# Kernel tuning notes

Hardware: AMD Instinct MI355X
Metric: run time of the kernel (lower is better)

The kernel has to match this reference:

```python
import jax, jax.numpy as jnp
import numpy as np

SEQ, IN_DIM, OUT_DIM = 8192, 1024, 1024

def setup_inputs() -> dict:
    key = jax.random.key(0)
    k1, k2, k3, k4 = jax.random.split(key, 4)
    inputs = jax.random.normal(k1, (SEQ, IN_DIM), dtype=jnp.float32)
    # torch.nn.Linear stores weight as [out_dim, in_dim]; y = x @ W.T
    w_query = jax.random.normal(k2, (OUT_DIM, IN_DIM), dtype=jnp.float32) * (1.0 / np.sqrt(IN_DIM))
    w_key = jax.random.normal(k3, (OUT_DIM, IN_DIM), dtype=jnp.float32) * (1.0 / np.sqrt(IN_DIM))
    w_value = jax.random.normal(k4, (OUT_DIM, IN_DIM), dtype=jnp.float32) * (1.0 / np.sqrt(IN_DIM))
    return {"inputs": inputs, "w_query": w_query, "w_key": w_key, "w_value": w_value}

def reference(inputs, w_query, w_key, w_value):
    # QKV projections: [S, D_out]
    q = inputs @ w_query.T
    k = inputs @ w_key.T
    v = inputs @ w_value.T
    scale = 1.0 / jnp.sqrt(jnp.asarray(k.shape[-1], dtype=q.dtype))
    scores = (q @ k.T) * scale  # [S, S]
    # causal mask: lower-triangular kept, upper set to -inf
    s = scores.shape[0]
    causal = jnp.tril(jnp.ones((s, s), dtype=bool))
    scores = jnp.where(causal, scores, -jnp.inf)
    attn = jax.nn.softmax(scores, axis=-1)
    return attn @ v
```

## Files before the change

kernel.cpp:

```cpp
#include <hip/hip_runtime.h>
#include <stdint.h>
#include <stddef.h>


#define SEQ   8192
#define DIM   1024

typedef __bf16 bf16x8 __attribute__((ext_vector_type(8)));
typedef float  f32x4  __attribute__((ext_vector_type(4)));
typedef uint16_t u16x8 __attribute__((ext_vector_type(8)));

#define MFMA16(a, b, c) __builtin_amdgcn_mfma_f32_16x16x32_bf16((a), (b), (c), 0, 0, 0)

__device__ __forceinline__ uint16_t f2bf(float f) {
  uint32_t u = __builtin_bit_cast(uint32_t, f);
  return (uint16_t)((u + 0x7fffu + ((u >> 16) & 1u)) >> 16);
}
__device__ __forceinline__ float bf2f(uint16_t h) {
  uint32_t u = ((uint32_t)h) << 16;
  return __builtin_bit_cast(float, u);
}

typedef const __attribute__((address_space(1))) uint32_t* gas_t;
typedef __attribute__((address_space(3))) uint32_t* las_t;
__device__ __forceinline__ void async16(const void* g, void* l) {
  __builtin_amdgcn_global_load_lds((gas_t)g, (las_t)l, 16, 0, 0);
}


__global__ __launch_bounds__(256) void cast_f32_bf16(const float* __restrict__ src,
                                                     uint16_t* __restrict__ dst, int n) {
  int i = (blockIdx.x * 256 + threadIdx.x) * 4;
  if (i + 3 < n) {
    float4 v = *(const float4*)(src + i);
    ushort4 o;
    o.x = f2bf(v.x); o.y = f2bf(v.y); o.z = f2bf(v.z); o.w = f2bf(v.w);
    *(ushort4*)(dst + i) = o;
  }
}

__global__ __launch_bounds__(256) void qkv_gemm(const uint16_t* __restrict__ A,
                                                const uint16_t* __restrict__ B,
                                                uint16_t* __restrict__ Qblk,
                                                uint16_t* __restrict__ Kblk,
                                                uint16_t* __restrict__ Vb) {
  __shared__ __align__(16) uint16_t As[128][72];
  __shared__ __align__(16) uint16_t Bs[128][72];
  const int t    = threadIdx.x;
  const int w    = t >> 6;
  const int lane = t & 63;
  const int lm   = lane & 15;
  const int qd   = lane >> 4;
  const int wrow = (w >> 1) * 64;
  const int wcol = (w & 1) * 64;
  const int rowbase = blockIdx.y * 128;
  const int colbase = blockIdx.x * 128;

  f32x4 acc[4][4] = {};

  for (int kb = 0; kb < DIM; kb += 64) {
    __syncthreads();
#pragma unroll
    for (int rep = 0; rep < 4; ++rep) {
      int i = rep * 256 + t;
      int r = i >> 3, c8 = i & 7;
      *(uint4*)(&As[r][c8 * 8]) =
          *(const uint4*)(A + (size_t)(rowbase + r) * DIM + kb + c8 * 8);
    }
#pragma unroll
    for (int rep = 0; rep < 4; ++rep) {
      int i = rep * 256 + t;
      int r = i >> 3, c8 = i & 7;
      *(uint4*)(&Bs[r][c8 * 8]) =
          *(const uint4*)(B + (size_t)(colbase + r) * DIM + kb + c8 * 8);
    }
    __syncthreads();
#pragma unroll
    for (int kc = 0; kc < 2; ++kc) {
      bf16x8 af[4], bfr[4];
#pragma unroll
      for (int mt = 0; mt < 4; ++mt)
        af[mt] = *(const bf16x8*)(&As[wrow + mt * 16 + lm][kc * 32 + qd * 8]);
#pragma unroll
      for (int nt = 0; nt < 4; ++nt)
        bfr[nt] = *(const bf16x8*)(&Bs[wcol + nt * 16 + lm][kc * 32 + qd * 8]);
#pragma unroll
      for (int mt = 0; mt < 4; ++mt)
#pragma unroll
        for (int nt = 0; nt < 4; ++nt)
          acc[mt][nt] = MFMA16(af[mt], bfr[nt], acc[mt][nt]);
    }
  }

#pragma unroll
  for (int mt = 0; mt < 4; ++mt)
#pragma unroll
    for (int nt = 0; nt < 4; ++nt)
#pragma unroll
      for (int r = 0; r < 4; ++r) {
        int m = rowbase + wrow + mt * 16 + qd * 4 + r;
        int n = colbase + wcol + nt * 16 + lm;
        uint16_t v = f2bf(acc[mt][nt][r]);
        int nn = n & 1023;
        if (n < 2048) {
          size_t off = (((size_t)(m >> 4) * 32 + (nn >> 5)) * 64 +
                        ((nn >> 3) & 3) * 16 + (m & 15)) * 8 + (nn & 7);
          if (n < 1024) Qblk[off] = v; else Kblk[off] = v;
        } else {
          Vb[(size_t)m * DIM + nn] = v;
        }
      }
}

__global__ __launch_bounds__(256) void transpose_v(const uint16_t* __restrict__ Vb,
                                                   uint16_t* __restrict__ Vblk) {
  __shared__ __align__(16) uint16_t tile[64][72];
  const int t  = threadIdx.x;
  const int mb = blockIdx.x * 64;
  const int db = blockIdx.y * 64;
#pragma unroll
  for (int rep = 0; rep < 2; ++rep) {
    int i = rep * 256 + t;
    int r = i >> 3, c = (i & 7) * 8;
    *(uint4*)(&tile[r][c]) = *(const uint4*)(Vb + (size_t)(mb + r) * DIM + db + c);
  }
  __syncthreads();
#pragma unroll
  for (int rep = 0; rep < 2; ++rep) {
    int i = rep * 256 + t;
    int d = i >> 3, mq = (i & 7) * 8;
    u16x8 v;
#pragma unroll
    for (int u = 0; u < 8; ++u) v[u] = tile[mq + u][d];
    int dg = db + d, kg = mb + mq;
    size_t off = (((size_t)(dg >> 4) * 256 + (kg >> 5)) * 64 +
                  ((kg >> 3) & 3) * 16 + (dg & 15)) * 8;
    *(u16x8*)(Vblk + off) = v;
  }
}

__global__ __launch_bounds__(512, 2) void attn_kernel(const uint16_t* __restrict__ Qblk,
                                                      const uint16_t* __restrict__ Kblk,
                                                      const uint16_t* __restrict__ Vblk,
                                                      uint16_t* __restrict__ P0,
                                                      uint16_t* __restrict__ P1,
                                                      float* __restrict__ Mm,
                                                      float* __restrict__ Ll) {
  __shared__ __align__(16) uint16_t Qs[32768];
  __shared__ __align__(16) uint16_t Pb[8192];
  __shared__ float smax[32][8];
  __shared__ float lsum[32][8];
  __shared__ float mrow[32];

  const int t    = threadIdx.x;
  const int w    = t >> 6;
  const int lane = t & 63;
  const int lm   = lane & 15;
  const int qd   = lane >> 4;
  const int par  = blockIdx.x & 1;
  const int p    = blockIdx.x >> 1;
  const float c1 = 0.045084220027780106f;

#pragma unroll 1
  for (int half = 0; half < 2; ++half) {
    const int tt   = half ? 255 - p : p;
    const int row0 = tt * 32;
    const int jn   = (tt >> 3) + 1;

    __syncthreads();
#pragma unroll
    for (int i = 0; i < 8; ++i)
      async16(Qblk + ((size_t)(tt * 64 + w * 8 + i)) * 512 + lane * 8,
              Qs + (w * 8 + i) * 512);
    __syncthreads();

    float m_run[2][4], l_run[2][4];
#pragma unroll
    for (int mt = 0; mt < 2; ++mt)
#pragma unroll
      for (int r = 0; r < 4; ++r) { m_run[mt][r] = -1e30f; l_run[mt][r] = 0.0f; }
    f32x4 o_acc[2][8] = {};

#pragma unroll 1
    for (int jg = par; jg < jn; jg += 2) {
      f32x4 sacc[2][2] = {};
      const uint16_t* kbp = Kblk + ((size_t)(jg * 16 + w * 2) * 32) * 512 + lane * 8;
      const uint16_t* qsp = Qs + lane * 8;
#pragma unroll 4
      for (int kb = 0; kb < 32; ++kb) {
        bf16x8 qf0 = *(const bf16x8*)(qsp + kb * 512);
        bf16x8 qf1 = *(const bf16x8*)(qsp + (32 + kb) * 512);
        bf16x8 kf0 = *(const bf16x8*)(kbp + (size_t)kb * 512);
        bf16x8 kf1 = *(const bf16x8*)(kbp + (size_t)(32 + kb) * 512);
        sacc[0][0] = MFMA16(qf0, kf0, sacc[0][0]);
        sacc[1][0] = MFMA16(qf1, kf0, sacc[1][0]);
        sacc[0][1] = MFMA16(qf0, kf1, sacc[0][1]);
        sacc[1][1] = MFMA16(qf1, kf1, sacc[1][1]);
      }

      if (jg == jn - 1) {
#pragma unroll
        for (int mt = 0; mt < 2; ++mt)
#pragma unroll
          for (int nt = 0; nt < 2; ++nt)
#pragma unroll
            for (int r = 0; r < 4; ++r) {
              int col = jg * 256 + w * 32 + nt * 16 + lm;
              int row = row0 + mt * 16 + qd * 4 + r;
              if (col > row) sacc[mt][nt][r] = -1e30f;
            }
      }

#pragma unroll
      for (int mt = 0; mt < 2; ++mt)
#pragma unroll
        for (int r = 0; r < 4; ++r) {
          float v = fmaxf(sacc[mt][0][r], sacc[mt][1][r]);
          v = fmaxf(v, __shfl_xor(v, 1));
          v = fmaxf(v, __shfl_xor(v, 2));
          v = fmaxf(v, __shfl_xor(v, 4));
          v = fmaxf(v, __shfl_xor(v, 8));
          if (lm == 0) smax[mt * 16 + qd * 4 + r][w] = v;
        }
      __syncthreads();

      float alpha[2][4], psum[2][4];
#pragma unroll
      for (int mt = 0; mt < 2; ++mt)
#pragma unroll
        for (int r = 0; r < 4; ++r) {
          int rl = mt * 16 + qd * 4 + r;
          float4 g0 = *(const float4*)&smax[rl][0];
          float4 g1 = *(const float4*)&smax[rl][4];
          float gm = fmaxf(fmaxf(fmaxf(g0.x, g0.y), fmaxf(g0.z, g0.w)),
                           fmaxf(fmaxf(g1.x, g1.y), fmaxf(g1.z, g1.w)));
          float mn = fmaxf(m_run[mt][r], gm);
          alpha[mt][r] = exp2f((m_run[mt][r] - mn) * c1);
          m_run[mt][r] = mn;
          psum[mt][r] = 0.0f;
        }
#pragma unroll
      for (int mt = 0; mt < 2; ++mt)
#pragma unroll
        for (int nt = 0; nt < 2; ++nt)
#pragma unroll
          for (int r = 0; r < 4; ++r) {
            float pv = exp2f((sacc[mt][nt][r] - m_run[mt][r]) * c1);
            psum[mt][r] += pv;
            Pb[((mt * 8 + w) * 64 + (nt * 2 + (lm >> 3)) * 16 + qd * 4 + r) * 8 + (lm & 7)] =
                f2bf(pv);
          }
#pragma unroll
      for (int mt = 0; mt < 2; ++mt)
#pragma unroll
        for (int r = 0; r < 4; ++r) {
          float s2 = psum[mt][r];
          s2 += __shfl_xor(s2, 1);
          s2 += __shfl_xor(s2, 2);
          s2 += __shfl_xor(s2, 4);
          s2 += __shfl_xor(s2, 8);
          l_run[mt][r] = l_run[mt][r] * alpha[mt][r] + s2;
        }
      __syncthreads();

#pragma unroll
      for (int mt = 0; mt < 2; ++mt)
#pragma unroll
        for (int dt = 0; dt < 8; ++dt)
#pragma unroll
          for (int r = 0; r < 4; ++r)
            o_acc[mt][dt][r] *= alpha[mt][r];

      const uint16_t* vbp = Vblk + ((size_t)(w * 8) * 256 + jg * 8) * 512 + lane * 8;
#pragma unroll 2
      for (int kc = 0; kc < 8; ++kc) {
        bf16x8 pf0 = *(const bf16x8*)(Pb + (kc * 64 + lane) * 8);
        bf16x8 pf1 = *(const bf16x8*)(Pb + ((8 + kc) * 64 + lane) * 8);
#pragma unroll
        for (int dt = 0; dt < 8; ++dt) {
          bf16x8 vf = *(const bf16x8*)(vbp + ((size_t)dt * 256 + kc) * 512);
          o_acc[0][dt] = MFMA16(pf0, vf, o_acc[0][dt]);
          o_acc[1][dt] = MFMA16(pf1, vf, o_acc[1][dt]);
        }
      }
    }

    if (lm == 0) {
#pragma unroll
      for (int mt = 0; mt < 2; ++mt)
#pragma unroll
        for (int r = 0; r < 4; ++r) {
          int rl = mt * 16 + qd * 4 + r;
          lsum[rl][w] = l_run[mt][r];
          if (w == 0) mrow[rl] = m_run[mt][r];
        }
    }
    __syncthreads();
    if (t < 32) {
      float4 a0 = *(const float4*)&lsum[t][0];
      float4 a1 = *(const float4*)&lsum[t][4];
      Mm[par * SEQ + row0 + t] = mrow[t];
      Ll[par * SEQ + row0 + t] = (a0.x + a0.y + a0.z + a0.w) + (a1.x + a1.y + a1.z + a1.w);
    }
    uint16_t* Pp = par ? P1 : P0;
#pragma unroll
    for (int mt = 0; mt < 2; ++mt)
#pragma unroll
      for (int dt = 0; dt < 8; ++dt)
#pragma unroll
        for (int r = 0; r < 4; ++r) {
          int row = row0 + mt * 16 + qd * 4 + r;
          int d   = w * 128 + dt * 16 + lm;
          Pp[(size_t)row * DIM + d] = f2bf(o_acc[mt][dt][r]);
        }
  }
}

__global__ __launch_bounds__(256) void merge_kernel(const uint16_t* __restrict__ P0,
                                                    const uint16_t* __restrict__ P1,
                                                    const float* __restrict__ Mm,
                                                    const float* __restrict__ Ll,
                                                    float* __restrict__ out) {
  const int row = blockIdx.x;
  const int d0  = threadIdx.x * 4;
  const float c1 = 0.045084220027780106f;
  float m0 = Mm[row], m1 = Mm[SEQ + row];
  float l0 = Ll[row], l1 = Ll[SEQ + row];
  float m  = fmaxf(m0, m1);
  float a0 = exp2f((m0 - m) * c1);
  float a1 = exp2f((m1 - m) * c1);
  float inv = 1.0f / (a0 * l0 + a1 * l1);
  ushort4 p0 = *(const ushort4*)(P0 + (size_t)row * DIM + d0);
  ushort4 p1 = *(const ushort4*)(P1 + (size_t)row * DIM + d0);
  float4 o;
  o.x = (a0 * bf2f(p0.x) + a1 * bf2f(p1.x)) * inv;
  o.y = (a0 * bf2f(p0.y) + a1 * bf2f(p1.y)) * inv;
  o.z = (a0 * bf2f(p0.z) + a1 * bf2f(p1.z)) * inv;
  o.w = (a0 * bf2f(p0.w) + a1 * bf2f(p1.w)) * inv;
  *(float4*)(out + (size_t)row * DIM + d0) = o;
}

extern "C" void kernel_launch(void* const* d_in, const int* in_sizes, int n_in,
                              void* d_out, int out_size, void* d_ws, size_t ws_size,
                              hipStream_t stream) {
  (void)in_sizes; (void)n_in; (void)out_size; (void)ws_size;
  const float* x  = (const float*)d_in[0];
  const float* wq = (const float*)d_in[1];
  const float* wk = (const float*)d_in[2];
  const float* wv = (const float*)d_in[3];
  float* out = (float*)d_out;

  char* ws = (char*)d_ws;
  uint16_t* Qblk = (uint16_t*)(ws);
  uint16_t* Kblk = (uint16_t*)(ws + 16777216);
  uint16_t* Vblk = (uint16_t*)(ws + 33554432);
  uint16_t* Vb   = (uint16_t*)(ws + 50331648);
  uint16_t* P0   = (uint16_t*)(ws + 50331648);
  uint16_t* xb   = (uint16_t*)(ws + 67108864);
  uint16_t* P1   = (uint16_t*)(ws + 67108864);
  uint16_t* wcat = (uint16_t*)(ws + 83886080);
  float*    Mm   = (float*)(ws + 83886080);
  float*    Ll   = (float*)(ws + 83886080 + 65536);

  cast_f32_bf16<<<8192, 256, 0, stream>>>(x,  xb,                   SEQ * DIM);
  cast_f32_bf16<<<1024, 256, 0, stream>>>(wq, wcat,                 DIM * DIM);
  cast_f32_bf16<<<1024, 256, 0, stream>>>(wk, wcat + DIM * DIM,     DIM * DIM);
  cast_f32_bf16<<<1024, 256, 0, stream>>>(wv, wcat + 2 * DIM * DIM, DIM * DIM);

  qkv_gemm<<<dim3(24, 64), 256, 0, stream>>>(xb, wcat, Qblk, Kblk, Vb);
  transpose_v<<<dim3(SEQ / 64, DIM / 64), 256, 0, stream>>>(Vb, Vblk);
  attn_kernel<<<256, 512, 0, stream>>>(Qblk, Kblk, Vblk, P0, P1, Mm, Ll);
  merge_kernel<<<SEQ, 256, 0, stream>>>(P0, P1, Mm, Ll, out);
}
```

Before: 557.6 us.

## Swizzle async LDS loads in QKV GEMM and halve attention P buffer

The QKV GEMM now loads A/B tiles directly into LDS via global_load_lds with an XOR-swizzled unpadded layout, avoiding register staging and bank conflicts. The attention kernel halves its P staging buffer by writing P in two phases (half the waves at a time) with extra barriers, merges stats arrays, reduces unrolling, and raises the launch-bounds occupancy hint to 4. This aims at lower LDS/register pressure and more resident waves, at the cost of additional synchronizations and possible register spills.

```diff
diff --git a/kernel.cpp b/kernel.cpp
--- a/kernel.cpp
+++ b/kernel.cpp
@@ -26,7 +26,6 @@
 __device__ __forceinline__ void async16(const void* g, void* l) {
   __builtin_amdgcn_global_load_lds((gas_t)g, (las_t)l, 16, 0, 0);
 }
-
 
 __global__ __launch_bounds__(256) void cast_f32_bf16(const float* __restrict__ src,
                                                      uint16_t* __restrict__ dst, int n) {
@@ -44,8 +43,8 @@
                                                 uint16_t* __restrict__ Qblk,
                                                 uint16_t* __restrict__ Kblk,
                                                 uint16_t* __restrict__ Vb) {
-  __shared__ __align__(16) uint16_t As[128][72];
-  __shared__ __align__(16) uint16_t Bs[128][72];
+  __shared__ __align__(16) uint16_t As[128 * 64];
+  __shared__ __align__(16) uint16_t Bs[128 * 64];
   const int t    = threadIdx.x;
   const int w    = t >> 6;
   const int lane = t & 63;
@@ -56,34 +55,33 @@
   const int rowbase = blockIdx.y * 128;
   const int colbase = blockIdx.x * 128;
 
+  const int lrow = lane >> 3;
+  const int lgrp = (lane & 7) ^ (lrow & 7);
+
   f32x4 acc[4][4] = {};
 
   for (int kb = 0; kb < DIM; kb += 64) {
     __syncthreads();
 #pragma unroll
     for (int rep = 0; rep < 4; ++rep) {
-      int i = rep * 256 + t;
-      int r = i >> 3, c8 = i & 7;
-      *(uint4*)(&As[r][c8 * 8]) =
-          *(const uint4*)(A + (size_t)(rowbase + r) * DIM + kb + c8 * 8);
-    }
-#pragma unroll
-    for (int rep = 0; rep < 4; ++rep) {
-      int i = rep * 256 + t;
-      int r = i >> 3, c8 = i & 7;
-      *(uint4*)(&Bs[r][c8 * 8]) =
-          *(const uint4*)(B + (size_t)(colbase + r) * DIM + kb + c8 * 8);
+      int r0 = rep * 32 + w * 8;
+      async16(A + (size_t)(rowbase + r0 + lrow) * DIM + kb + lgrp * 8, As + r0 * 64);
+      async16(B + (size_t)(colbase + r0 + lrow) * DIM + kb + lgrp * 8, Bs + r0 * 64);
     }
     __syncthreads();
 #pragma unroll
     for (int kc = 0; kc < 2; ++kc) {
       bf16x8 af[4], bfr[4];
 #pragma unroll
-      for (int mt = 0; mt < 4; ++mt)
-        af[mt] = *(const bf16x8*)(&As[wrow + mt * 16 + lm][kc * 32 + qd * 8]);
-#pragma unroll
-      for (int nt = 0; nt < 4; ++nt)
-        bfr[nt] = *(const bf16x8*)(&Bs[wcol + nt * 16 + lm][kc * 32 + qd * 8]);
+      for (int mt = 0; mt < 4; ++mt) {
+        int r = wrow + mt * 16 + lm;
+        af[mt] = *(const bf16x8*)(As + r * 64 + (((kc * 4 + qd) ^ (lm & 7)) * 8));
+      }
+#pragma unroll
+      for (int nt = 0; nt < 4; ++nt) {
+        int r = wcol + nt * 16 + lm;
+        bfr[nt] = *(const bf16x8*)(Bs + r * 64 + (((kc * 4 + qd) ^ (lm & 7)) * 8));
+      }
 #pragma unroll
       for (int mt = 0; mt < 4; ++mt)
 #pragma unroll
@@ -139,7 +137,7 @@
   }
 }
 
-__global__ __launch_bounds__(512, 2) void attn_kernel(const uint16_t* __restrict__ Qblk,
+__global__ __launch_bounds__(512, 4) void attn_kernel(const uint16_t* __restrict__ Qblk,
                                                       const uint16_t* __restrict__ Kblk,
                                                       const uint16_t* __restrict__ Vblk,
                                                       uint16_t* __restrict__ P0,
@@ -147,9 +145,8 @@
                                                       float* __restrict__ Mm,
                                                       float* __restrict__ Ll) {
   __shared__ __align__(16) uint16_t Qs[32768];
-  __shared__ __align__(16) uint16_t Pb[8192];
-  __shared__ float smax[32][8];
-  __shared__ float lsum[32][8];
+  __shared__ __align__(16) uint16_t Pb[4096];
+  __shared__ float stats[32][8];
   __shared__ float mrow[32];
 
   const int t    = threadIdx.x;
@@ -157,6 +154,8 @@
   const int lane = t & 63;
   const int lm   = lane & 15;
   const int qd   = lane >> 4;
+  const int wp   = w >> 2;
+  const int wk   = w & 3;
   const int par  = blockIdx.x & 1;
   const int p    = blockIdx.x >> 1;
   const float c1 = 0.045084220027780106f;
@@ -186,7 +185,7 @@
       f32x4 sacc[2][2] = {};
       const uint16_t* kbp = Kblk + ((size_t)(jg * 16 + w * 2) * 32) * 512 + lane * 8;
       const uint16_t* qsp = Qs + lane * 8;
-#pragma unroll 4
+#pragma unroll 2
       for (int kb = 0; kb < 32; ++kb) {
         bf16x8 qf0 = *(const bf16x8*)(qsp + kb * 512);
         bf16x8 qf1 = *(const bf16x8*)(qsp + (32 + kb) * 512);
@@ -220,18 +219,19 @@
           v = fmaxf(v, __shfl_xor(v, 2));
           v = fmaxf(v, __shfl_xor(v, 4));
           v = fmaxf(v, __shfl_xor(v, 8));
-          if (lm == 0) smax[mt * 16 + qd * 4 + r][w] = v;
+          if (lm == 0) stats[mt * 16 + qd * 4 + r][w] = v;
         }
       __syncthreads();
 
       float alpha[2][4], psum[2][4];
+      uint16_t pvh[2][2][4];
 #pragma unroll
       for (int mt = 0; mt < 2; ++mt)
 #pragma unroll
         for (int r = 0; r < 4; ++r) {
           int rl = mt * 16 + qd * 4 + r;
-          float4 g0 = *(const float4*)&smax[rl][0];
-          float4 g1 = *(const float4*)&smax[rl][4];
+          float4 g0 = *(const float4*)&stats[rl][0];
+          float4 g1 = *(const float4*)&stats[rl][4];
           float gm = fmaxf(fmaxf(fmaxf(g0.x, g0.y), fmaxf(g0.z, g0.w)),
                            fmaxf(fmaxf(g1.x, g1.y), fmaxf(g1.z, g1.w)));
           float mn = fmaxf(m_run[mt][r], gm);
@@ -247,8 +247,7 @@
           for (int r = 0; r < 4; ++r) {
             float pv = exp2f((sacc[mt][nt][r] - m_run[mt][r]) * c1);
             psum[mt][r] += pv;
-            Pb[((mt * 8 + w) * 64 + (nt * 2 + (lm >> 3)) * 16 + qd * 4 + r) * 8 + (lm & 7)] =
-                f2bf(pv);
+            pvh[mt][nt][r] = f2bf(pv);
           }
 #pragma unroll
       for (int mt = 0; mt < 2; ++mt)
@@ -261,6 +260,16 @@
           s2 += __shfl_xor(s2, 8);
           l_run[mt][r] = l_run[mt][r] * alpha[mt][r] + s2;
         }
+      if (wp == 0) {
+#pragma unroll
+        for (int mt = 0; mt < 2; ++mt)
+#pragma unroll
+          for (int nt = 0; nt < 2; ++nt)
+#pragma unroll
+            for (int r = 0; r < 4; ++r)
+              Pb[((mt * 4 + wk) * 64 + (nt * 2 + (lm >> 3)) * 16 + qd * 4 + r) * 8 +
+                 (lm & 7)] = pvh[mt][nt][r];
+      }
       __syncthreads();
 
 #pragma unroll
@@ -273,9 +282,9 @@
 
       const uint16_t* vbp = Vblk + ((size_t)(w * 8) * 256 + jg * 8) * 512 + lane * 8;
 #pragma unroll 2
-      for (int kc = 0; kc < 8; ++kc) {
+      for (int kc = 0; kc < 4; ++kc) {
         bf16x8 pf0 = *(const bf16x8*)(Pb + (kc * 64 + lane) * 8);
-        bf16x8 pf1 = *(const bf16x8*)(Pb + ((8 + kc) * 64 + lane) * 8);
+        bf16x8 pf1 = *(const bf16x8*)(Pb + ((4 + kc) * 64 + lane) * 8);
 #pragma unroll
         for (int dt = 0; dt < 8; ++dt) {
           bf16x8 vf = *(const bf16x8*)(vbp + ((size_t)dt * 256 + kc) * 512);
@@ -283,6 +292,30 @@
           o_acc[1][dt] = MFMA16(pf1, vf, o_acc[1][dt]);
         }
       }
+      __syncthreads();
+      if (wp == 1) {
+#pragma unroll
+        for (int mt = 0; mt < 2; ++mt)
+#pragma unroll
+          for (int nt = 0; nt < 2; ++nt)
+#pragma unroll
+            for (int r = 0; r < 4; ++r)
+              Pb[((mt * 4 + wk) * 64 + (nt * 2 + (lm >> 3)) * 16 + qd * 4 + r) * 8 +
+                 (lm & 7)] = pvh[mt][nt][r];
+      }
+      __syncthreads();
+
+#pragma unroll 2
+      for (int kc = 0; kc < 4; ++kc) {
+        bf16x8 pf0 = *(const bf16x8*)(Pb + (kc * 64 + lane) * 8);
+        bf16x8 pf1 = *(const bf16x8*)(Pb + ((4 + kc) * 64 + lane) * 8);
+#pragma unroll
+        for (int dt = 0; dt < 8; ++dt) {
+          bf16x8 vf = *(const bf16x8*)(vbp + ((size_t)dt * 256 + 4 + kc) * 512);
+          o_acc[0][dt] = MFMA16(pf0, vf, o_acc[0][dt]);
+          o_acc[1][dt] = MFMA16(pf1, vf, o_acc[1][dt]);
+        }
+      }
     }
 
     if (lm == 0) {
@@ -291,14 +324,14 @@
 #pragma unroll
         for (int r = 0; r < 4; ++r) {
           int rl = mt * 16 + qd * 4 + r;
-          lsum[rl][w] = l_run[mt][r];
+          stats[rl][w] = l_run[mt][r];
           if (w == 0) mrow[rl] = m_run[mt][r];
         }
     }
     __syncthreads();
     if (t < 32) {
-      float4 a0 = *(const float4*)&lsum[t][0];
-      float4 a1 = *(const float4*)&lsum[t][4];
+      float4 a0 = *(const float4*)&stats[t][0];
+      float4 a1 = *(const float4*)&stats[t][4];
       Mm[par * SEQ + row0 + t] = mrow[t];
       Ll[par * SEQ + row0 + t] = (a0.x + a0.y + a0.z + a0.w) + (a1.x + a1.y + a1.z + a1.w);
     }
```

Result: slower. 958.5 us (+71.9%).
